# Optimization experiments

Measured on AMD Instinct MI355X. Metric: run time of the kernel, lower is better.

Reference implementation:

```python
import jax, jax.numpy as jnp
import numpy as np

B, IN, H = 4096, 512, 1024
ALPHA, RHO = 0.001, 0.05

def setup_inputs() -> dict:
    key = jax.random.key(0)
    ks = jax.random.split(key, 9)
    inp = jax.random.normal(ks[0], (B, IN), dtype=jnp.float32)
    time = jax.random.uniform(ks[1], (B, 1), dtype=jnp.float32) * 100.0
    hx = jax.random.normal(ks[2], (B, H), dtype=jnp.float32)
    cx = jax.random.normal(ks[3], (B, H), dtype=jnp.float32)
    # params (match torch init scales loosely)
    Wxh_w = jax.random.normal(ks[4], (4 * H, IN), dtype=jnp.float32) / np.sqrt(IN)
    Wxh_b = jnp.zeros((4 * H,), dtype=jnp.float32)
    Whh_w = jax.random.normal(ks[5], (4 * H, H), dtype=jnp.float32) / np.sqrt(H)
    tau = jax.random.normal(ks[6], (H,), dtype=jnp.float32) * 0.5 + 5.0
    s = jax.random.uniform(ks[7], (H,), dtype=jnp.float32) * tau
    alpha = jnp.array([ALPHA], dtype=jnp.float32)
    rho = jnp.array([RHO], dtype=jnp.float32)
    return {"input": inp, "time": time, "hx": hx, "cx": cx,
            "Wxh_w": Wxh_w, "Wxh_b": Wxh_b, "Whh_w": Whh_w,
            "tau": tau, "s": s, "alpha": alpha, "rho": rho}

def _time_gate(time, s, tau, alpha, rho):
    # phi: [B, H] (time [B,1] broadcast against s/tau [H])
    phi = jnp.fmod(time - s, tau) / tau
    k = jnp.where(phi < rho / 2.0, 2.0 * phi / rho,
        jnp.where(phi < rho, 2.0 - 2.0 * phi / rho, alpha * phi))
    # computed under torch.no_grad() in the original
    return jax.lax.stop_gradient(k)

def reference(input, time, hx, cx, Wxh_w, Wxh_b, Whh_w, tau, s, alpha, rho):
    gates = input @ Wxh_w.T + Wxh_b + hx @ Whh_w.T  # [B, 4H]
    i, f, g, o = jnp.split(gates, 4, axis=1)
    k = _time_gate(time, s, tau, alpha, rho)
    ft = jax.nn.sigmoid(f + 1.0 - k)
    it = jax.nn.sigmoid(i) * k
    gt = jnp.tanh(g) * k
    ot = jax.nn.sigmoid(o) * k
    cy = ft * cx + it * gt
    hy = ot * jnp.tanh(cy)
    return (hy, cy)
```

## Files before the change

### kernel.cpp

```cpp
#include <hip/hip_runtime.h>

#define AS1 __attribute__((address_space(1)))
#define AS3 __attribute__((address_space(3)))

typedef _Float16 half_t;
typedef __attribute__((ext_vector_type(8))) _Float16 f16x8;
typedef __attribute__((ext_vector_type(4))) float f32x4;

static constexpr int Bsz = 4096;
static constexpr int INs = 512;
static constexpr int Hs  = 1024;
static constexpr int BM  = 128;
static constexpr int BH  = 32;
static constexpr int BK  = 64;
static constexpr int NIT = INs / BK + Hs / BK;

static constexpr size_t XN  = (size_t)Bsz * INs;
static constexpr size_t HXN = (size_t)Bsz * Hs;
static constexpr size_t WXN = (size_t)4 * Hs * INs;
static constexpr size_t WHN = (size_t)4 * Hs * Hs;
static constexpr size_t OFF_X  = 0;
static constexpr size_t OFF_HX = XN;
static constexpr size_t OFF_WX = XN + HXN;
static constexpr size_t OFF_WH = XN + HXN + WXN;
static constexpr size_t TOT    = XN + HXN + WXN + WHN;

__device__ __forceinline__ float sigm(float x) {
  return 1.0f / (1.0f + __expf(-x));
}
__device__ __forceinline__ float tanh_fast(float x) {
  const float e = __expf(2.0f * x);
  return 1.0f - 2.0f / (e + 1.0f);
}

__global__ __launch_bounds__(256)
void cvt_kernel(const float* __restrict__ x, const float* __restrict__ hx,
                const float* __restrict__ wx, const float* __restrict__ wh,
                half_t* __restrict__ ws) {
  const size_t cid = (size_t)blockIdx.x * 256 + threadIdx.x;
  const size_t e = cid * 8;
  const float* src; size_t off;
  if (e < OFF_HX)      { src = x;  off = e - OFF_X; }
  else if (e < OFF_WX) { src = hx; off = e - OFF_HX; }
  else if (e < OFF_WH) { src = wx; off = e - OFF_WX; }
  else                 { src = wh; off = e - OFF_WH; }
  const f32x4 a = *(const f32x4*)(src + off);
  const f32x4 b = *(const f32x4*)(src + off + 4);
  f16x8 o;
  o[0]=(half_t)a[0]; o[1]=(half_t)a[1]; o[2]=(half_t)a[2]; o[3]=(half_t)a[3];
  o[4]=(half_t)b[0]; o[5]=(half_t)b[1]; o[6]=(half_t)b[2]; o[7]=(half_t)b[3];
  *(f16x8*)(ws + e) = o;
}

__global__ __launch_bounds__(256, 4)
void plstm_gemm(const half_t* __restrict__ xin,
                const half_t* __restrict__ hxp,
                const float* __restrict__ cxp,
                const half_t* __restrict__ wxh,
                const float* __restrict__ biasp,
                const half_t* __restrict__ whh,
                const float* __restrict__ timep,
                const float* __restrict__ taup,
                const float* __restrict__ sp,
                const float* __restrict__ alphap,
                const float* __restrict__ rhop,
                float* __restrict__ outp)
{
  __shared__ half_t As[BM * BK];
  __shared__ half_t Bs[BM * BK];

  const int tid  = threadIdx.x;
  const int w    = tid >> 6;
  const int lane = tid & 63;
  const int l15  = lane & 15;
  const int grp  = lane >> 4;
  const int wr   = w >> 1;
  const int wc   = w & 1;

  const int wg = blockIdx.x + (blockIdx.y << 5);
  const int xk = wg & 7;
  const int q  = wg >> 3;
  const int m0 = (q >> 2) * BM;
  const int h0 = ((xk << 2) + (q & 3)) * BH;

  f32x4 acc[4][4] = {};

  const int ldr = tid >> 3;
  const int ldc = tid & 7;

  for (int it = 0; it < NIT; ++it) {
    const bool p1 = it >= INs / BK;
    const half_t* Ap = p1 ? hxp : xin;
    const half_t* Wp = p1 ? whh : wxh;
    const int Ka = p1 ? Hs : INs;
    const int k0 = (p1 ? (it - INs / BK) : it) * BK;
    #pragma unroll
    for (int i = 0; i < 4; ++i) {
      const int e    = i * 32 + ldr;
      const int gc8  = ldc ^ (e & 7);
      const int wrow = ((e >> 4) & 3) * Hs + h0 + ((e >> 6) << 4) + (e & 15);
      const half_t* ga = Ap + (size_t)(m0 + e) * Ka + (k0 + gc8 * 8);
      __builtin_amdgcn_global_load_lds((AS1 void*)ga,
                                       (AS3 void*)(As + (e * 8 + ldc) * 8), 16, 0, 0);
      const half_t* gw = Wp + (size_t)wrow * Ka + (k0 + gc8 * 8);
      __builtin_amdgcn_global_load_lds((AS1 void*)gw,
                                       (AS3 void*)(Bs + (e * 8 + ldc) * 8), 16, 0, 0);
    }
    __syncthreads();

    #pragma unroll
    for (int kk = 0; kk < 2; ++kk) {
      const int c8x = kk * 4 + grp;
      f16x8 af[4], bfr[4];
      #pragma unroll
      for (int mt = 0; mt < 4; ++mt) {
        const int e = wr * 64 + mt * 16 + l15;
        af[mt] = *(const f16x8*)(As + (e * 8 + (c8x ^ (l15 & 7))) * 8);
      }
      #pragma unroll
      for (int nt = 0; nt < 4; ++nt) {
        const int e = wc * 64 + nt * 16 + l15;
        bfr[nt] = *(const f16x8*)(Bs + (e * 8 + (c8x ^ (l15 & 7))) * 8);
      }
      #pragma unroll
      for (int mt = 0; mt < 4; ++mt)
        #pragma unroll
        for (int nt = 0; nt < 4; ++nt)
          acc[mt][nt] = __builtin_amdgcn_mfma_f32_16x16x32_f16(
              af[mt], bfr[nt], acc[mt][nt], 0, 0, 0);
    }
    __syncthreads();
  }

  const int h = h0 + wc * 16 + l15;
  const float bi  = biasp[h];
  const float bfv = biasp[Hs + h];
  const float bg  = biasp[2 * Hs + h];
  const float bo  = biasp[3 * Hs + h];
  const float sv = sp[h], tauv = taup[h];
  const float alphav = alphap[0], rhov = rhop[0], rh = 0.5f * rhov;
  const float rtau   = 1.0f / tauv;
  const float tworho = 2.0f / rhov;

  #pragma unroll
  for (int mt = 0; mt < 4; ++mt) {
    const f32x4 t4 = *(const f32x4*)(timep + m0 + wr * 64 + mt * 16 + grp * 4);
    #pragma unroll
    for (int r = 0; r < 4; ++r) {
      const int brow = m0 + wr * 64 + mt * 16 + grp * 4 + r;
      const float qv  = (t4[r] - sv) * rtau;
      const float phi = qv - truncf(qv);
      const float kv  = phi < rh   ? phi * tworho
                      : (phi < rhov ? 2.0f - phi * tworho
                                    : alphav * phi);

      const float iv = acc[mt][0][r] + bi;
      const float fv = acc[mt][1][r] + bfv;
      const float gv = acc[mt][2][r] + bg;
      const float ov = acc[mt][3][r] + bo;
      const float cxv = cxp[(size_t)brow * Hs + h];
      const float ft = sigm(fv + 1.0f - kv);
      const float it2 = sigm(iv) * kv;
      const float gt = tanh_fast(gv) * kv;
      const float ot = sigm(ov) * kv;
      const float cy = ft * cxv + it2 * gt;
      const float hy = ot * tanh_fast(cy);

      outp[(size_t)brow * Hs + h] = hy;
      outp[(size_t)Bsz * Hs + (size_t)brow * Hs + h] = cy;
    }
  }
}

__global__ __launch_bounds__(256, 3)
void plstm_gemm_f32(const float* __restrict__ xin, const float* __restrict__ timep,
                    const float* __restrict__ hxp, const float* __restrict__ cxp,
                    const float* __restrict__ wxh, const float* __restrict__ biasp,
                    const float* __restrict__ whh, const float* __restrict__ taup,
                    const float* __restrict__ sp, const float* __restrict__ alphap,
                    const float* __restrict__ rhop, float* __restrict__ outp)
{
  __shared__ half_t As[BM * BK];
  __shared__ half_t Bs[BM * BK];

  const int tid  = threadIdx.x;
  const int w    = tid >> 6;
  const int lane = tid & 63;
  const int l15  = lane & 15;
  const int grp  = lane >> 4;
  const int wr   = w >> 1;
  const int wc   = w & 1;

  const int m0 = blockIdx.x * BM;
  const int h0 = blockIdx.y * BH;

  f32x4 acc[4][4] = {};
  const int ldr = tid >> 3;
  const int ldc = tid & 7;

  for (int it = 0; it < NIT; ++it) {
    const bool p1 = it >= INs / BK;
    const float* Ap = p1 ? hxp : xin;
    const float* Wp = p1 ? whh : wxh;
    const int Ka = p1 ? Hs : INs;
    const int k0 = (p1 ? (it - INs / BK) : it) * BK;
    #pragma unroll
    for (int i = 0; i < 4; ++i) {
      const int e    = i * 32 + ldr;
      const int gc8  = ldc ^ (e & 7);
      const int wrow = ((e >> 4) & 3) * Hs + h0 + ((e >> 6) << 4) + (e & 15);
      const float* ga = Ap + (size_t)(m0 + e) * Ka + (k0 + gc8 * 8);
      const f32x4 a0v = *(const f32x4*)ga, a1v = *(const f32x4*)(ga + 4);
      f16x8 pa;
      pa[0]=(half_t)a0v[0]; pa[1]=(half_t)a0v[1]; pa[2]=(half_t)a0v[2]; pa[3]=(half_t)a0v[3];
      pa[4]=(half_t)a1v[0]; pa[5]=(half_t)a1v[1]; pa[6]=(half_t)a1v[2]; pa[7]=(half_t)a1v[3];
      *(f16x8*)(As + (e * 8 + ldc) * 8) = pa;
      const float* gw = Wp + (size_t)wrow * Ka + (k0 + gc8 * 8);
      const f32x4 b0v = *(const f32x4*)gw, b1v = *(const f32x4*)(gw + 4);
      f16x8 pb;
      pb[0]=(half_t)b0v[0]; pb[1]=(half_t)b0v[1]; pb[2]=(half_t)b0v[2]; pb[3]=(half_t)b0v[3];
      pb[4]=(half_t)b1v[0]; pb[5]=(half_t)b1v[1]; pb[6]=(half_t)b1v[2]; pb[7]=(half_t)b1v[3];
      *(f16x8*)(Bs + (e * 8 + ldc) * 8) = pb;
    }
    __syncthreads();
    #pragma unroll
    for (int kk = 0; kk < 2; ++kk) {
      const int c8x = kk * 4 + grp;
      f16x8 af[4], bfr[4];
      #pragma unroll
      for (int mt = 0; mt < 4; ++mt) {
        const int e = wr * 64 + mt * 16 + l15;
        af[mt] = *(const f16x8*)(As + (e * 8 + (c8x ^ (l15 & 7))) * 8);
      }
      #pragma unroll
      for (int nt = 0; nt < 4; ++nt) {
        const int e = wc * 64 + nt * 16 + l15;
        bfr[nt] = *(const f16x8*)(Bs + (e * 8 + (c8x ^ (l15 & 7))) * 8);
      }
      #pragma unroll
      for (int mt = 0; mt < 4; ++mt)
        #pragma unroll
        for (int nt = 0; nt < 4; ++nt)
          acc[mt][nt] = __builtin_amdgcn_mfma_f32_16x16x32_f16(
              af[mt], bfr[nt], acc[mt][nt], 0, 0, 0);
    }
    __syncthreads();
  }

  const int h = h0 + wc * 16 + l15;
  const float bi  = biasp[h];
  const float bfv = biasp[Hs + h];
  const float bg  = biasp[2 * Hs + h];
  const float bo  = biasp[3 * Hs + h];
  const float sv = sp[h], tauv = taup[h];
  const float alphav = alphap[0], rhov = rhop[0], rh = 0.5f * rhov;
  const float rtau   = 1.0f / tauv;
  const float tworho = 2.0f / rhov;

  #pragma unroll
  for (int mt = 0; mt < 4; ++mt) {
    const f32x4 t4 = *(const f32x4*)(timep + m0 + wr * 64 + mt * 16 + grp * 4);
    #pragma unroll
    for (int r = 0; r < 4; ++r) {
      const int brow = m0 + wr * 64 + mt * 16 + grp * 4 + r;
      const float qv  = (t4[r] - sv) * rtau;
      const float phi = qv - truncf(qv);
      const float kv  = phi < rh   ? phi * tworho
                      : (phi < rhov ? 2.0f - phi * tworho
                                    : alphav * phi);
      const float iv = acc[mt][0][r] + bi;
      const float fv = acc[mt][1][r] + bfv;
      const float gv = acc[mt][2][r] + bg;
      const float ov = acc[mt][3][r] + bo;
      const float cxv = cxp[(size_t)brow * Hs + h];
      const float ft = sigm(fv + 1.0f - kv);
      const float it2 = sigm(iv) * kv;
      const float gt = tanh_fast(gv) * kv;
      const float ot = sigm(ov) * kv;
      const float cy = ft * cxv + it2 * gt;
      const float hy = ot * tanh_fast(cy);
      outp[(size_t)brow * Hs + h] = hy;
      outp[(size_t)Bsz * Hs + (size_t)brow * Hs + h] = cy;
    }
  }
}

extern "C" void kernel_launch(void* const* d_in, const int* in_sizes, int n_in,
                              void* d_out, int out_size, void* d_ws, size_t ws_size,
                              hipStream_t stream) {
  (void)in_sizes; (void)n_in; (void)out_size;
  const float* xin   = (const float*)d_in[0];
  const float* timep = (const float*)d_in[1];
  const float* hxp   = (const float*)d_in[2];
  const float* cxp   = (const float*)d_in[3];
  const float* wxh   = (const float*)d_in[4];
  const float* biasp = (const float*)d_in[5];
  const float* whh   = (const float*)d_in[6];
  const float* taup  = (const float*)d_in[7];
  const float* sp    = (const float*)d_in[8];
  const float* alphap= (const float*)d_in[9];
  const float* rhop  = (const float*)d_in[10];
  float* outp = (float*)d_out;

  dim3 grid(Bsz / BM, Hs / BH);
  if (ws_size >= TOT * sizeof(half_t)) {
    half_t* ws = (half_t*)d_ws;
    cvt_kernel<<<(int)(TOT / 8 / 256), 256, 0, stream>>>(xin, hxp, wxh, whh, ws);
    plstm_gemm<<<grid, 256, 0, stream>>>(
        ws + OFF_X, ws + OFF_HX, cxp, ws + OFF_WX, biasp, ws + OFF_WH,
        timep, taup, sp, alphap, rhop, outp);
  } else {
    plstm_gemm_f32<<<grid, 256, 0, stream>>>(
        xin, timep, hxp, cxp, wxh, biasp, whh,
        taup, sp, alphap, rhop, outp);
  }
}
```

Baseline: 178.6 us.

## Double-buffer LDS tiles in fp16 PLSTM GEMM to overlap loads with MFMA

Splits the main loop into stage and compute lambdas over two LDS buffers, so the global_load_lds for the next K-tile is issued before the MFMAs on the current tile, and one barrier per iteration is removed. LDS use doubles and launch bounds drop from 4 to 2 blocks per CU, which lowers occupancy. The f32 fallback kernel only renames its B buffer. There is a risk that the async LDS loads are not waited on correctly before the barrier.

Result: slower. 197.3 us (+10.5%).

```diff
diff --git a/kernel.cpp b/kernel.cpp
--- a/kernel.cpp
+++ b/kernel.cpp
@@ -52,7 +52,7 @@
   *(f16x8*)(ws + e) = o;
 }
 
-__global__ __launch_bounds__(256, 4)
+__global__ __launch_bounds__(256, 2)
 void plstm_gemm(const half_t* __restrict__ xin,
                 const half_t* __restrict__ hxp,
                 const float* __restrict__ cxp,
@@ -66,8 +66,8 @@
                 const float* __restrict__ rhop,
                 float* __restrict__ outp)
 {
-  __shared__ half_t As[BM * BK];
-  __shared__ half_t Bs[BM * BK];
+  __shared__ half_t As[2][BM * BK];
+  __shared__ half_t Bs[2][BM * BK];
 
   const int tid  = threadIdx.x;
   const int w    = tid >> 6;
@@ -88,12 +88,12 @@
   const int ldr = tid >> 3;
   const int ldc = tid & 7;
 
-  for (int it = 0; it < NIT; ++it) {
-    const bool p1 = it >= INs / BK;
+  auto stage = [&](int t, int p) {
+    const bool p1 = t >= INs / BK;
     const half_t* Ap = p1 ? hxp : xin;
     const half_t* Wp = p1 ? whh : wxh;
     const int Ka = p1 ? Hs : INs;
-    const int k0 = (p1 ? (it - INs / BK) : it) * BK;
+    const int k0 = (p1 ? (t - INs / BK) : t) * BK;
     #pragma unroll
     for (int i = 0; i < 4; ++i) {
       const int e    = i * 32 + ldr;
@@ -101,13 +101,14 @@
       const int wrow = ((e >> 4) & 3) * Hs + h0 + ((e >> 6) << 4) + (e & 15);
       const half_t* ga = Ap + (size_t)(m0 + e) * Ka + (k0 + gc8 * 8);
       __builtin_amdgcn_global_load_lds((AS1 void*)ga,
-                                       (AS3 void*)(As + (e * 8 + ldc) * 8), 16, 0, 0);
+          (AS3 void*)(As[p] + (e * 8 + ldc) * 8), 16, 0, 0);
       const half_t* gw = Wp + (size_t)wrow * Ka + (k0 + gc8 * 8);
       __builtin_amdgcn_global_load_lds((AS1 void*)gw,
-                                       (AS3 void*)(Bs + (e * 8 + ldc) * 8), 16, 0, 0);
-    }
-    __syncthreads();
-
+          (AS3 void*)(Bs[p] + (e * 8 + ldc) * 8), 16, 0, 0);
+    }
+  };
+
+  auto compute = [&](int p) {
     #pragma unroll
     for (int kk = 0; kk < 2; ++kk) {
       const int c8x = kk * 4 + grp;
@@ -115,12 +116,12 @@
       #pragma unroll
       for (int mt = 0; mt < 4; ++mt) {
         const int e = wr * 64 + mt * 16 + l15;
-        af[mt] = *(const f16x8*)(As + (e * 8 + (c8x ^ (l15 & 7))) * 8);
+        af[mt] = *(const f16x8*)(As[p] + (e * 8 + (c8x ^ (l15 & 7))) * 8);
       }
       #pragma unroll
       for (int nt = 0; nt < 4; ++nt) {
         const int e = wc * 64 + nt * 16 + l15;
-        bfr[nt] = *(const f16x8*)(Bs + (e * 8 + (c8x ^ (l15 & 7))) * 8);
+        bfr[nt] = *(const f16x8*)(Bs[p] + (e * 8 + (c8x ^ (l15 & 7))) * 8);
       }
       #pragma unroll
       for (int mt = 0; mt < 4; ++mt)
@@ -129,8 +130,18 @@
           acc[mt][nt] = __builtin_amdgcn_mfma_f32_16x16x32_f16(
               af[mt], bfr[nt], acc[mt][nt], 0, 0, 0);
     }
+  };
+
+  stage(0, 0);
+  __syncthreads();
+
+  #pragma unroll 1
+  for (int it = 0; it < NIT - 1; ++it) {
+    stage(it + 1, (it + 1) & 1);
+    compute(it & 1);
     __syncthreads();
   }
+  compute((NIT - 1) & 1);
 
   const int h = h0 + wc * 16 + l15;
   const float bi  = biasp[h];
@@ -181,7 +192,7 @@
                     const float* __restrict__ rhop, float* __restrict__ outp)
 {
   __shared__ half_t As[BM * BK];
-  __shared__ half_t Bs[BM * BK];
+  __shared__ half_t Bsf[BM * BK];
 
   const int tid  = threadIdx.x;
   const int w    = tid >> 6;
@@ -220,7 +231,7 @@
       f16x8 pb;
       pb[0]=(half_t)b0v[0]; pb[1]=(half_t)b0v[1]; pb[2]=(half_t)b0v[2]; pb[3]=(half_t)b0v[3];
       pb[4]=(half_t)b1v[0]; pb[5]=(half_t)b1v[1]; pb[6]=(half_t)b1v[2]; pb[7]=(half_t)b1v[3];
-      *(f16x8*)(Bs + (e * 8 + ldc) * 8) = pb;
+      *(f16x8*)(Bsf + (e * 8 + ldc) * 8) = pb;
     }
     __syncthreads();
     #pragma unroll
@@ -235,7 +246,7 @@
       #pragma unroll
       for (int nt = 0; nt < 4; ++nt) {
         const int e = wc * 64 + nt * 16 + l15;
-        bfr[nt] = *(const f16x8*)(Bs + (e * 8 + (c8x ^ (l15 & 7))) * 8);
+        bfr[nt] = *(const f16x8*)(Bsf + (e * 8 + (c8x ^ (l15 & 7))) * 8);
       }
       #pragma unroll
       for (int mt = 0; mt < 4; ++mt)
```
